# Optimization experiments

Measured on AMD Instinct MI355X. Metric: run time of the kernel, lower is better.

Reference implementation:

```python
import jax, jax.numpy as jnp
import numpy as np

B, T, D, H = 4, 1024, 1024, 16


def setup_inputs() -> dict:
    key = jax.random.key(0)
    ks = jax.random.split(key, 6)
    s = 0.02  # small init so softmax is well-conditioned
    return {
        "x": jax.random.normal(ks[0], (B, T, D), jnp.float32),
        "position_embedding": jax.random.normal(ks[1], (B, T, D), jnp.float32),
        "Wc": jax.random.normal(ks[2], (2 * D, D), jnp.float32) * s,
        "bc": jnp.zeros((2 * D,), jnp.float32),
        "Wp": jax.random.normal(ks[3], (D, D), jnp.float32) * s,
        "bp": jnp.zeros((D,), jnp.float32),
        "Wo": jax.random.normal(ks[4], (D, D), jnp.float32) * s,
        "bo": jnp.zeros((D,), jnp.float32),
        "num_heads": H,
    }


def reference(x, position_embedding, Wc, bc, Wp, bp, Wo, bo, num_heads):
    b, t, d = x.shape
    h = num_heads
    hd = d // h
    scale = hd ** -0.5
    # content projection -> q, k  (value reuses content k, as in the original)
    cqk = (x @ Wc.T + bc).reshape(b, t, 2, h, hd)
    q = cqk[:, :, 0]  # [B,T,H,hd]
    k = cqk[:, :, 1]  # [B,T,H,hd]
    # position keys
    pk = (position_embedding @ Wp.T + bp).reshape(b, t, h, hd)
    # dual-stream scores: content-content + content-position
    scores = (jnp.einsum('bqhd,bkhd->bhqk', q, k)
              + jnp.einsum('bqhd,bkhd->bhqk', q, pk)) * scale
    attn = jax.nn.softmax(scores, axis=-1)  # dropout is identity in eval
    out = jnp.einsum('bhqk,bkhd->bqhd', attn, k).reshape(b, t, d)
    return out @ Wo.T + bo, attn
```

## Files before the change

### kernel.cpp

```cpp
#include <hip/hip_runtime.h>
#include <hip/hip_bf16.h>

#define BB 4
#define TT 1024
#define DD 1024
#define HH 16
#define HDIM 64
#define MM (BB*TT)

typedef unsigned short u16;
typedef __attribute__((ext_vector_type(8))) short bf16x8;
typedef __attribute__((ext_vector_type(8))) _Float16 f16x8;
typedef __attribute__((ext_vector_type(4))) float f32x4;
typedef __attribute__((ext_vector_type(4))) unsigned short u16x4;

__device__ __forceinline__ u16 f2bf(float f) {
    union { float f; unsigned u; } v; v.f = f;
    return (u16)((v.u + 0x7fffu + ((v.u >> 16) & 1u)) >> 16);
}
__device__ __forceinline__ float bf2f(u16 h) {
    union { unsigned u; float f; } v; v.u = ((unsigned)h) << 16; return v.f;
}
__device__ __forceinline__ u16 f2h(float f) {
    union { _Float16 h; u16 u; } v; v.h = (_Float16)f;
    return v.u;
}

__device__ __forceinline__ void gload16(const void* g, void* l) {
    __builtin_amdgcn_global_load_lds(
        (const __attribute__((address_space(1))) unsigned int*)g,
        (__attribute__((address_space(3))) unsigned int*)l, 16, 0, 0);
}

template<bool TO_FP16>
__global__ __launch_bounds__(256)
void cvt_kernel(const float* __restrict__ src, u16* __restrict__ dst)
{
    const size_t i = ((size_t)blockIdx.x * 256 + threadIdx.x) * 4;
    const float4 v = *(const float4*)&src[i];
    u16x4 o;
    if constexpr (TO_FP16) {
        o[0] = f2h(v.x); o[1] = f2h(v.y); o[2] = f2h(v.z); o[3] = f2h(v.w);
    } else {
        o[0] = f2bf(v.x); o[1] = f2bf(v.y); o[2] = f2bf(v.z); o[3] = f2bf(v.w);
    }
    *(u16x4*)&dst[i] = o;
}

__global__ __launch_bounds__(256)
void ktrans_kernel(const u16* __restrict__ k16, u16* __restrict__ k16T)
{
    __shared__ u16 tmp[64][72];
    const int tc = blockIdx.x, h = blockIdx.y, b = blockIdx.z;
    const size_t hb = ((size_t)(b * HH + h)) << 16;
    const int tid = threadIdx.x;
    const int sr = tid >> 2, sc = (tid & 3) * 8;
    *(bf16x8*)&tmp[sr][sc]      = *(const bf16x8*)&k16[hb + (size_t)(tc * 64 + sr) * HDIM + sc];
    *(bf16x8*)&tmp[sr][sc + 32] = *(const bf16x8*)&k16[hb + (size_t)(tc * 64 + sr) * HDIM + sc + 32];
    __syncthreads();
#pragma unroll
    for (int half = 0; half < 2; ++half) {
        bf16x8 v;
#pragma unroll
        for (int j = 0; j < 8; ++j) v[j] = (short)tmp[sc + half * 32 + j][sr];
        *(bf16x8*)&k16T[hb + (size_t)sr * TT + tc * 64 + sc + half * 32] = v;
    }
}

template<bool FP16, int MODE>
__global__ __launch_bounds__(256)
void gemm_mfma(const u16* __restrict__ Ah, const u16* __restrict__ Bh,
               const float* __restrict__ bias,
               float* __restrict__ dstF, u16* __restrict__ dstH1,
               u16* __restrict__ dstH2, const float* __restrict__ kaux,
               const int M, const int N, const int K)
{
    __shared__ u16 As[128][64];
    __shared__ u16 Bs[128][64];

    const int tid  = threadIdx.x;
    const int w    = tid >> 6;
    const int lane = tid & 63;
    const int lg   = lane >> 4;
    const int lr   = lane & 15;
    const int wr   = w >> 1, wc = w & 1;
    const int m0   = blockIdx.y * 128, n0 = blockIdx.x * 128;

    const f32x4 zero = {0.f, 0.f, 0.f, 0.f};
    f32x4 acc[4][4];
#pragma unroll
    for (int i = 0; i < 4; ++i)
#pragma unroll
        for (int j = 0; j < 4; ++j) acc[i][j] = zero;

    const int srow = tid >> 3;
    const int scol = (tid & 7) * 8;
    const int ldr  = w << 3;

    for (int k0 = 0; k0 < K; k0 += 64) {
        __syncthreads();
#pragma unroll
        for (int i = 0; i < 4; ++i) {
            const size_t ga = (size_t)(m0 + i * 32 + srow) * K + k0 + scol;
            const size_t gb = (size_t)(n0 + i * 32 + srow) * K + k0 + scol;
            gload16(&Ah[ga], &As[i * 32 + ldr][0]);
            gload16(&Bh[gb], &Bs[i * 32 + ldr][0]);
        }
        __syncthreads();
#pragma unroll
        for (int kk = 0; kk < 2; ++kk) {
            const int koff = kk * 32 + lg * 8;
#pragma unroll
            for (int mf = 0; mf < 4; ++mf) {
#pragma unroll
                for (int nf = 0; nf < 4; ++nf) {
                    if constexpr (FP16) {
                        const f16x8 a = *(const f16x8*)&As[wr * 64 + mf * 16 + lr][koff];
                        const f16x8 b = *(const f16x8*)&Bs[wc * 64 + nf * 16 + lr][koff];
                        acc[mf][nf] = __builtin_amdgcn_mfma_f32_16x16x32_f16(a, b, acc[mf][nf], 0, 0, 0);
                    } else {
                        const bf16x8 a = *(const bf16x8*)&As[wr * 64 + mf * 16 + lr][koff];
                        const bf16x8 b = *(const bf16x8*)&Bs[wc * 64 + nf * 16 + lr][koff];
                        acc[mf][nf] = __builtin_amdgcn_mfma_f32_16x16x32_bf16(a, b, acc[mf][nf], 0, 0, 0);
                    }
                }
            }
        }
    }

#pragma unroll
    for (int mf = 0; mf < 4; ++mf)
#pragma unroll
        for (int nf = 0; nf < 4; ++nf)
#pragma unroll
            for (int j = 0; j < 4; ++j) {
                const int gm = m0 + wr * 64 + mf * 16 + lg * 4 + j;
                const int gn = n0 + wc * 64 + nf * 16 + lr;
                const float v = acc[mf][nf][j] + bias[gn];
                if constexpr (MODE == 0) {
                    const int bb = gm >> 10, t = gm & 1023;
                    const int c = gn >> 10, hh = (gn & 1023) >> 6, d = gn & 63;
                    const size_t idx = ((((size_t)bb * HH + hh) << 10) + t) * HDIM + d;
                    if (c == 0) dstH1[idx] = f2bf(v * 0.125f);
                    else { dstF[idx] = v; dstH2[idx] = f2bf(v); }
                } else if constexpr (MODE == 1) {
                    const int bb = gm >> 10, t = gm & 1023;
                    const int hh = gn >> 6, d = gn & 63;
                    const size_t idx = ((((size_t)bb * HH + hh) << 10) + t) * HDIM + d;
                    dstH1[idx] = f2bf(v + kaux[idx]);
                } else {
                    dstF[(size_t)gm * N + gn] = v;
                }
            }
}

__global__ __launch_bounds__(256)
void attn_mfma(const u16* __restrict__ qg, const u16* __restrict__ kTg,
               const u16* __restrict__ kpg,
               float* __restrict__ attn, u16* __restrict__ ch)
{
    __shared__ u16 kp_s[2][64][72];
    __shared__ u16 kT_s[2][64][72];
    __shared__ u16 P_s[4][16][72];

    const int tid  = threadIdx.x;
    const int w    = tid >> 6;
    const int lane = tid & 63;
    const int lg   = lane >> 4;
    const int lr   = lane & 15;
    const int q0   = blockIdx.x * 64;
    const int h = blockIdx.y, b = blockIdx.z;
    const size_t hb = ((size_t)(b * HH + h)) << 16;

    bf16x8 qf0, qf1;
    {
        const size_t base = hb + (size_t)(q0 + w * 16 + lr) * HDIM + lg * 8;
        qf0 = *(const bf16x8*)&qg[base];
        qf1 = *(const bf16x8*)&qg[base + 32];
    }

    const int sr = tid >> 2;
    const int sc = (tid & 3) * 8;
    bf16x8 ra, rb, rc, rd;

    ra = *(const bf16x8*)&kpg[hb + (size_t)sr * HDIM + sc];
    rb = *(const bf16x8*)&kpg[hb + (size_t)sr * HDIM + sc + 32];
    *(bf16x8*)&kp_s[0][sr][sc]      = ra;
    *(bf16x8*)&kp_s[0][sr][sc + 32] = rb;
    __syncthreads();

    float rs[4] = {0.f, 0.f, 0.f, 0.f};
    for (int t = 0; t < TT / 64; ++t) {
        const int cur = t & 1;
        if (t < 15) {
            const size_t nb = hb + (size_t)((t + 1) * 64 + sr) * HDIM;
            ra = *(const bf16x8*)&kpg[nb + sc];
            rb = *(const bf16x8*)&kpg[nb + sc + 32];
        }
#pragma unroll
        for (int ct = 0; ct < 4; ++ct) {
            f32x4 acc = {0.f, 0.f, 0.f, 0.f};
            const bf16x8 b0 = *(const bf16x8*)&kp_s[cur][ct * 16 + lr][lg * 8];
            const bf16x8 b1 = *(const bf16x8*)&kp_s[cur][ct * 16 + lr][lg * 8 + 32];
            acc = __builtin_amdgcn_mfma_f32_16x16x32_bf16(qf0, b0, acc, 0, 0, 0);
            acc = __builtin_amdgcn_mfma_f32_16x16x32_bf16(qf1, b1, acc, 0, 0, 0);
#pragma unroll
            for (int j = 0; j < 4; ++j) rs[j] += __expf(acc[j]);
        }
        if (t < 15) {
            *(bf16x8*)&kp_s[cur ^ 1][sr][sc]      = ra;
            *(bf16x8*)&kp_s[cur ^ 1][sr][sc + 32] = rb;
        }
        __syncthreads();
    }

    ra = *(const bf16x8*)&kpg[hb + (size_t)sr * HDIM + sc];
    rb = *(const bf16x8*)&kpg[hb + (size_t)sr * HDIM + sc + 32];
    rc = *(const bf16x8*)&kTg[hb + (size_t)sr * TT + sc];
    rd = *(const bf16x8*)&kTg[hb + (size_t)sr * TT + sc + 32];
#pragma unroll
    for (int off = 1; off < 16; off <<= 1) {
#pragma unroll
        for (int j = 0; j < 4; ++j) rs[j] += __shfl_xor(rs[j], off);
    }
    float ri[4];
#pragma unroll
    for (int j = 0; j < 4; ++j) ri[j] = 1.f / rs[j];
    *(bf16x8*)&kp_s[0][sr][sc]      = ra;
    *(bf16x8*)&kp_s[0][sr][sc + 32] = rb;
    *(bf16x8*)&kT_s[0][sr][sc]      = rc;
    *(bf16x8*)&kT_s[0][sr][sc + 32] = rd;
    __syncthreads();

    f32x4 cacc[4] = {{0,0,0,0},{0,0,0,0},{0,0,0,0},{0,0,0,0}};
    const size_t abase = ((((size_t)b * HH + h) << 10) + q0 + w * 16) << 10;

    for (int t = 0; t < TT / 64; ++t) {
        const int cur = t & 1;
        if (t < 15) {
            const size_t nb = hb + (size_t)((t + 1) * 64 + sr) * HDIM;
            ra = *(const bf16x8*)&kpg[nb + sc];
            rb = *(const bf16x8*)&kpg[nb + sc + 32];
            const size_t tb = hb + (size_t)sr * TT + (t + 1) * 64;
            rc = *(const bf16x8*)&kTg[tb + sc];
            rd = *(const bf16x8*)&kTg[tb + sc + 32];
        }
#pragma unroll
        for (int ct = 0; ct < 4; ++ct) {
            f32x4 acc = {0.f, 0.f, 0.f, 0.f};
            const bf16x8 b0 = *(const bf16x8*)&kp_s[cur][ct * 16 + lr][lg * 8];
            const bf16x8 b1 = *(const bf16x8*)&kp_s[cur][ct * 16 + lr][lg * 8 + 32];
            acc = __builtin_amdgcn_mfma_f32_16x16x32_bf16(qf0, b0, acc, 0, 0, 0);
            acc = __builtin_amdgcn_mfma_f32_16x16x32_bf16(qf1, b1, acc, 0, 0, 0);
            const int col = t * 64 + ct * 16 + lr;
#pragma unroll
            for (int j = 0; j < 4; ++j) {
                const float p = __expf(acc[j]) * ri[j];
                attn[abase + (size_t)(lg * 4 + j) * TT + col] = p;
                P_s[w][lg * 4 + j][ct * 16 + lr] = f2bf(p);
            }
        }
        asm volatile("s_waitcnt lgkmcnt(0)" ::: "memory");
        const bf16x8 pa0 = *(const bf16x8*)&P_s[w][lr][lg * 8];
        const bf16x8 pa1 = *(const bf16x8*)&P_s[w][lr][lg * 8 + 32];
#pragma unroll
        for (int dt = 0; dt < 4; ++dt) {
            const bf16x8 kb0 = *(const bf16x8*)&kT_s[cur][dt * 16 + lr][lg * 8];
            const bf16x8 kb1 = *(const bf16x8*)&kT_s[cur][dt * 16 + lr][lg * 8 + 32];
            cacc[dt] = __builtin_amdgcn_mfma_f32_16x16x32_bf16(pa0, kb0, cacc[dt], 0, 0, 0);
            cacc[dt] = __builtin_amdgcn_mfma_f32_16x16x32_bf16(pa1, kb1, cacc[dt], 0, 0, 0);
        }
        if (t < 15) {
            *(bf16x8*)&kp_s[cur ^ 1][sr][sc]      = ra;
            *(bf16x8*)&kp_s[cur ^ 1][sr][sc + 32] = rb;
            *(bf16x8*)&kT_s[cur ^ 1][sr][sc]      = rc;
            *(bf16x8*)&kT_s[cur ^ 1][sr][sc + 32] = rd;
        }
        __syncthreads();
    }

#pragma unroll
    for (int dt = 0; dt < 4; ++dt)
#pragma unroll
        for (int j = 0; j < 4; ++j) {
            const int qr = q0 + w * 16 + lg * 4 + j;
            ch[(((size_t)b << 10) + qr) * DD + h * HDIM + dt * 16 + lr] = f2bf(cacc[dt][j]);
        }
}

extern "C" void kernel_launch(void* const* d_in, const int* in_sizes, int n_in,
                              void* d_out, int out_size, void* d_ws, size_t ws_size,
                              hipStream_t stream)
{
    const float* x  = (const float*)d_in[0];
    const float* pe = (const float*)d_in[1];
    const float* Wc = (const float*)d_in[2];
    const float* bc = (const float*)d_in[3];
    const float* Wp = (const float*)d_in[4];
    const float* bp = (const float*)d_in[5];
    const float* Wo = (const float*)d_in[6];
    const float* bo = (const float*)d_in[7];

    float* out  = (float*)d_out;
    float* attn = out + (size_t)MM * DD;

    char* ws = (char*)d_ws;
    float* kf32 = (float*)(ws);
    u16* q16  = (u16*)(ws + ((size_t)16 << 20));
    u16* k16  = (u16*)(ws + ((size_t)24 << 20));
    u16* kp16 = (u16*)(ws + ((size_t)32 << 20));
    u16* x16  = (u16*)(ws + ((size_t)40 << 20));
    u16* Wc16 = (u16*)(ws + ((size_t)56 << 20));
    u16* k16T = (u16*)(ws + ((size_t)56 << 20));
    u16* pe16 = x16;
    u16* Wp16 = (u16*)(ws + ((size_t)24 << 20));
    u16* chh  = x16;
    u16* Wo16 = (u16*)(ws + ((size_t)48 << 20));

    cvt_kernel<true><<<4096, 256, 0, stream>>>(x, x16);
    cvt_kernel<true><<<2048, 256, 0, stream>>>(Wc, Wc16);
    gemm_mfma<true, 0><<<dim3(16, 32), 256, 0, stream>>>(
        x16, Wc16, bc, kf32, q16, k16, nullptr, MM, 2048, DD);
    ktrans_kernel<<<dim3(16, HH, BB), 256, 0, stream>>>(k16, k16T);
    cvt_kernel<true><<<4096, 256, 0, stream>>>(pe, pe16);
    cvt_kernel<true><<<1024, 256, 0, stream>>>(Wp, Wp16);
    gemm_mfma<true, 1><<<dim3(8, 32), 256, 0, stream>>>(
        pe16, Wp16, bp, nullptr, kp16, nullptr, kf32, MM, 1024, DD);
    attn_mfma<<<dim3(TT / 64, HH, BB), 256, 0, stream>>>(
        q16, k16T, kp16, attn, chh);
    cvt_kernel<false><<<1024, 256, 0, stream>>>(Wo, Wo16);
    gemm_mfma<false, 2><<<dim3(8, 32), 256, 0, stream>>>(
        chh, Wo16, bo, out, nullptr, nullptr, nullptr, MM, 1024, DD);
}
```

Before: 202.8 us.

## Merge conversion kernels, drop fp32 k buffer, remap attention grid, nontemporal attn stores

Merges the five fp32-to-half conversion launches into two multi-segment kernels to reduce launch count. Stops writing an fp32 copy of the content key and adds the bf16 key inside the position GEMM epilogue instead, which cuts memory traffic but adds a bf16 rounding step before the sum. The attention grid is flattened and remapped so consecutive blocks spread across heads, likely to improve placement across chiplets or caches. The attention probability matrix is written with nontemporal stores so it does not pollute the cache.

```diff
diff --git a/kernel.cpp b/kernel.cpp
--- a/kernel.cpp
+++ b/kernel.cpp
@@ -32,19 +32,36 @@
         (__attribute__((address_space(3))) unsigned int*)l, 16, 0, 0);
 }
 
-template<bool TO_FP16>
-__global__ __launch_bounds__(256)
-void cvt_kernel(const float* __restrict__ src, u16* __restrict__ dst)
-{
-    const size_t i = ((size_t)blockIdx.x * 256 + threadIdx.x) * 4;
+__device__ __forceinline__ void cvt_body(const float* __restrict__ src,
+                                         u16* __restrict__ dst,
+                                         int bid, bool to_fp16)
+{
+    const size_t i = ((size_t)bid * 256 + threadIdx.x) * 4;
     const float4 v = *(const float4*)&src[i];
     u16x4 o;
-    if constexpr (TO_FP16) {
-        o[0] = f2h(v.x); o[1] = f2h(v.y); o[2] = f2h(v.z); o[3] = f2h(v.w);
-    } else {
-        o[0] = f2bf(v.x); o[1] = f2bf(v.y); o[2] = f2bf(v.z); o[3] = f2bf(v.w);
-    }
+    if (to_fp16) { o[0] = f2h(v.x); o[1] = f2h(v.y); o[2] = f2h(v.z); o[3] = f2h(v.w); }
+    else         { o[0] = f2bf(v.x); o[1] = f2bf(v.y); o[2] = f2bf(v.z); o[3] = f2bf(v.w); }
     *(u16x4*)&dst[i] = o;
+}
+
+__global__ __launch_bounds__(256)
+void cvt1_kernel(const float* __restrict__ x, u16* __restrict__ x16,
+                 const float* __restrict__ Wc, u16* __restrict__ Wc16)
+{
+    const int bid = blockIdx.x;
+    if (bid < 4096) cvt_body(x, x16, bid, true);
+    else            cvt_body(Wc, Wc16, bid - 4096, true);
+}
+
+__global__ __launch_bounds__(256)
+void cvt2_kernel(const float* __restrict__ pe, u16* __restrict__ pe16,
+                 const float* __restrict__ Wp, u16* __restrict__ Wp16,
+                 const float* __restrict__ Wo, u16* __restrict__ Wo16)
+{
+    const int bid = blockIdx.x;
+    if (bid < 4096)      cvt_body(pe, pe16, bid, true);
+    else if (bid < 5120) cvt_body(Wp, Wp16, bid - 4096, true);
+    else                 cvt_body(Wo, Wo16, bid - 5120, false);
 }
 
 __global__ __launch_bounds__(256)
@@ -72,7 +89,7 @@
 void gemm_mfma(const u16* __restrict__ Ah, const u16* __restrict__ Bh,
                const float* __restrict__ bias,
                float* __restrict__ dstF, u16* __restrict__ dstH1,
-               u16* __restrict__ dstH2, const float* __restrict__ kaux,
+               const u16* __restrict__ kaux16,
                const int M, const int N, const int K)
 {
     __shared__ u16 As[128][64];
@@ -142,12 +159,12 @@
                     const int c = gn >> 10, hh = (gn & 1023) >> 6, d = gn & 63;
                     const size_t idx = ((((size_t)bb * HH + hh) << 10) + t) * HDIM + d;
                     if (c == 0) dstH1[idx] = f2bf(v * 0.125f);
-                    else { dstF[idx] = v; dstH2[idx] = f2bf(v); }
+                    else        ((u16*)dstF)[idx] = f2bf(v);
                 } else if constexpr (MODE == 1) {
                     const int bb = gm >> 10, t = gm & 1023;
                     const int hh = gn >> 6, d = gn & 63;
                     const size_t idx = ((((size_t)bb * HH + hh) << 10) + t) * HDIM + d;
-                    dstH1[idx] = f2bf(v + kaux[idx]);
+                    dstH1[idx] = f2bf(v + bf2f(kaux16[idx]));
                 } else {
                     dstF[(size_t)gm * N + gn] = v;
                 }
@@ -168,8 +185,13 @@
     const int lane = tid & 63;
     const int lg   = lane >> 4;
     const int lr   = lane & 15;
-    const int q0   = blockIdx.x * 64;
-    const int h = blockIdx.y, b = blockIdx.z;
+
+    const int fid = blockIdx.x;
+    const int c   = fid & 7;
+    const int s   = fid >> 3;
+    const int g   = c + 8 * (s >> 4);
+    const int q0  = (s & 15) * 64;
+    const int b   = g >> 4, h = g & 15;
     const size_t hb = ((size_t)(b * HH + h)) << 16;
 
     bf16x8 qf0, qf1;
@@ -256,7 +278,7 @@
 #pragma unroll
             for (int j = 0; j < 4; ++j) {
                 const float p = __expf(acc[j]) * ri[j];
-                attn[abase + (size_t)(lg * 4 + j) * TT + col] = p;
+                __builtin_nontemporal_store(p, &attn[abase + (size_t)(lg * 4 + j) * TT + col]);
                 P_s[w][lg * 4 + j][ct * 16 + lr] = f2bf(p);
             }
         }
@@ -305,30 +327,25 @@
     float* attn = out + (size_t)MM * DD;
 
     char* ws = (char*)d_ws;
-    float* kf32 = (float*)(ws);
+    u16* Wp16 = (u16*)(ws);
     u16* q16  = (u16*)(ws + ((size_t)16 << 20));
     u16* k16  = (u16*)(ws + ((size_t)24 << 20));
     u16* kp16 = (u16*)(ws + ((size_t)32 << 20));
     u16* x16  = (u16*)(ws + ((size_t)40 << 20));
+    u16* Wo16 = (u16*)(ws + ((size_t)48 << 20));
     u16* Wc16 = (u16*)(ws + ((size_t)56 << 20));
     u16* k16T = (u16*)(ws + ((size_t)56 << 20));
     u16* pe16 = x16;
-    u16* Wp16 = (u16*)(ws + ((size_t)24 << 20));
     u16* chh  = x16;
-    u16* Wo16 = (u16*)(ws + ((size_t)48 << 20));
-
-    cvt_kernel<true><<<4096, 256, 0, stream>>>(x, x16);
-    cvt_kernel<true><<<2048, 256, 0, stream>>>(Wc, Wc16);
+
+    cvt1_kernel<<<6144, 256, 0, stream>>>(x, x16, Wc, Wc16);
     gemm_mfma<true, 0><<<dim3(16, 32), 256, 0, stream>>>(
-        x16, Wc16, bc, kf32, q16, k16, nullptr, MM, 2048, DD);
+        x16, Wc16, bc, (float*)k16, q16, nullptr, MM, 2048, DD);
     ktrans_kernel<<<dim3(16, HH, BB), 256, 0, stream>>>(k16, k16T);
-    cvt_kernel<true><<<4096, 256, 0, stream>>>(pe, pe16);
-    cvt_kernel<true><<<1024, 256, 0, stream>>>(Wp, Wp16);
+    cvt2_kernel<<<6144, 256, 0, stream>>>(pe, pe16, Wp, Wp16, Wo, Wo16);
     gemm_mfma<true, 1><<<dim3(8, 32), 256, 0, stream>>>(
-        pe16, Wp16, bp, nullptr, kp16, nullptr, kf32, MM, 1024, DD);
-    attn_mfma<<<dim3(TT / 64, HH, BB), 256, 0, stream>>>(
-        q16, k16T, kp16, attn, chh);
-    cvt_kernel<false><<<1024, 256, 0, stream>>>(Wo, Wo16);
+        pe16, Wp16, bp, nullptr, kp16, k16, MM, 1024, DD);
+    attn_mfma<<<1024, 256, 0, stream>>>(q16, k16T, kp16, attn, chh);
     gemm_mfma<false, 2><<<dim3(8, 32), 256, 0, stream>>>(
-        chh, Wo16, bo, out, nullptr, nullptr, nullptr, MM, 1024, DD);
-}
+        chh, Wo16, bo, out, nullptr, nullptr, MM, 1024, DD);
+}
```

After: 195.8 us. 1.04x faster.
